# Optimization experiments

Measured on AMD Instinct MI355X. Metric: run time of the kernel, lower is better.

Reference implementation:

```python
import jax, jax.numpy as jnp
import numpy as np

B, N, D, H = 2, 256, 512, 8
DK = D // H


def _lin(x, w, b):
    # torch nn.Linear: y = x @ W.T + b, W is [out, in]
    return jnp.matmul(x, w.T) + b


def setup_inputs() -> dict:
    key = jax.random.key(0)
    ks = jax.random.split(key, 12)
    std = 0.02
    inp = {
        "x": jax.random.normal(ks[0], (B, N, D), jnp.float32),
        "batched_graphs": jax.random.normal(ks[1], (B, N, N, D), jnp.float32) * std,
        "mask": jnp.zeros((B, N, N), dtype=bool),
    }
    names = ["wq", "wk", "wv", "wo", "wl", "wr", "wrk", "wrv"]
    for i, n in enumerate(names):
        inp[n] = jax.random.normal(ks[2 + i], (D, D), jnp.float32) * std
        inp["b" + n[1:]] = jnp.zeros((D,), jnp.float32)
    return inp


def reference(x, batched_graphs, mask,
              wq, bq, wk, bk, wv, bv, wo, bo,
              wl, bl, wr, br, wrk, brk, wrv, brv):
    # update_relations: per-edge key/value maps
    graphs_k = _lin(batched_graphs, wrk, brk).reshape(B, N, N, H, DK)
    graphs_v = _lin(batched_graphs, wrv, brv).reshape(B, N, N, H, DK)

    query = _lin(x, wq, bq).reshape(B, N, H, DK)
    key_ = _lin(x, wk, bk).reshape(B, N, H, DK)
    value = _lin(x, wv, bv).reshape(B, N, H, DK)

    scores_k = jnp.einsum("bxhd,byhd->bxyh", query, key_)
    scores_g = jnp.einsum("bxhd,bxyhd->bxyh", query, graphs_k)
    scores = (scores_k + scores_g) / np.sqrt(DK).astype(np.float32)
    scores = jnp.where(mask[..., None], jnp.float32(-1e9), scores)
    p_attn = jax.nn.softmax(scores, axis=2)  # over key nodes y

    x_v = jnp.einsum("bxyh,byhd->bxhd", p_attn, value)
    x_g = jnp.einsum("bxyh,bxyhd->bxhd", p_attn, graphs_v)
    out = (x_v + x_g).reshape(B, N, D)

    # relation update: outer sum of left/right projections
    x_left = _lin(out, wl, bl)[:, :, None, :]   # [B,N,1,D]
    x_right = _lin(out, wr, br)[:, None, :, :]  # [B,1,N,D]
    new_graphs = x_left + x_right               # [B,N,N,D]

    return _lin(out, wo, bo), new_graphs
```

## Files before the change

### kernel.cpp

```cpp
#include <hip/hip_runtime.h>

#define BB 2
#define NN 256
#define DD 512
#define HH 8

typedef float f4raw __attribute__((ext_vector_type(4)));

__device__ __forceinline__ float dot4(float4 a, float4 b) {
    return a.x*b.x + a.y*b.y + a.z*b.z + a.w*b.w;
}

__device__ __forceinline__ float4 f4fma(float s, float4 a, float4 acc) {
    acc.x += s * a.x; acc.y += s * a.y; acc.z += s * a.z; acc.w += s * a.w;
    return acc;
}

__device__ __forceinline__ void gload_lds16(const void* g, void* l) {
    __builtin_amdgcn_global_load_lds(
        (const __attribute__((address_space(1))) unsigned int*)g,
        (__attribute__((address_space(3))) unsigned int*)l, 16, 0, 0);
}

__device__ __forceinline__ void stage_swz(const char* rowbase, float4* dst, int w, int lane) {
    #pragma unroll
    for (int j = 0; j < 4; ++j) {
        const int f0 = w * 256 + j * 64;
        const int y = f0 >> 7;
        const int c = (f0 & 127) + lane;
        gload_lds16(rowbase + (size_t)y * 2048 + ((size_t)(c ^ y) << 4), &dst[f0]);
    }
}

__global__ __launch_bounds__(256) void kProj(
    const float* __restrict__ in_,
    const float* __restrict__ w0, const float* __restrict__ b0,
    const float* __restrict__ w1, const float* __restrict__ b1,
    const float* __restrict__ w2, const float* __restrict__ b2,
    float* __restrict__ o0, float* __restrict__ o1, float* __restrict__ o2)
{
    __shared__ float4 xs[2][32 * 17];
    __shared__ float4 ws[2][32 * 17];

    const int t = threadIdx.x;
    const int blk = blockIdx.x;
    const int proj = blk >> 8;
    const int rem = blk & 255;
    const int row0 = (rem >> 4) * 32;
    const int col0 = (rem & 15) * 32;

    const float* W; const float* Bp; float* O;
    if (proj == 0)      { W = w0; Bp = b0; O = o0; }
    else if (proj == 1) { W = w1; Bp = b1; O = o1; }
    else                { W = w2; Bp = b2; O = o2; }

    const int sr0 = t >> 4,          se0 = t & 15;
    const int sr1 = (t + 256) >> 4,  se1 = t & 15;
    const float4* X4 = (const float4*)in_;
    const float4* W4 = (const float4*)W;

    float4 rx0 = X4[(size_t)(row0 + sr0) * 128 + se0];
    float4 rx1 = X4[(size_t)(row0 + sr1) * 128 + se1];
    float4 rw0 = W4[(size_t)(col0 + sr0) * 128 + se0];
    float4 rw1 = W4[(size_t)(col0 + sr1) * 128 + se1];
    xs[0][sr0 * 17 + se0] = rx0;
    xs[0][sr1 * 17 + se1] = rx1;
    ws[0][sr0 * 17 + se0] = rw0;
    ws[0][sr1 * 17 + se1] = rw1;

    const int ty = t >> 4, tx = t & 15;
    const int ra = 2 * ty, ca = 2 * tx;
    float a00 = 0, a01 = 0, a10 = 0, a11 = 0;

    for (int q = 0; q < 8; ++q) {
        __syncthreads();
        const int cur = q & 1;
        if (q < 7) {
            const int koff = (q + 1) * 16;
            rx0 = X4[(size_t)(row0 + sr0) * 128 + koff + se0];
            rx1 = X4[(size_t)(row0 + sr1) * 128 + koff + se1];
            rw0 = W4[(size_t)(col0 + sr0) * 128 + koff + se0];
            rw1 = W4[(size_t)(col0 + sr1) * 128 + koff + se1];
        }
        const float4* xb = xs[cur];
        const float4* wb = ws[cur];
        #pragma unroll
        for (int e4 = 0; e4 < 16; ++e4) {
            const float4 x0 = xb[ra * 17 + e4];
            const float4 x1 = xb[(ra + 1) * 17 + e4];
            const float4 v0 = wb[ca * 17 + e4];
            const float4 v1 = wb[(ca + 1) * 17 + e4];
            a00 += dot4(x0, v0); a01 += dot4(x0, v1);
            a10 += dot4(x1, v0); a11 += dot4(x1, v1);
        }
        if (q < 7) {
            const int nxt = cur ^ 1;
            xs[nxt][sr0 * 17 + se0] = rx0;
            xs[nxt][sr1 * 17 + se1] = rx1;
            ws[nxt][sr0 * 17 + se0] = rw0;
            ws[nxt][sr1 * 17 + se1] = rw1;
        }
    }

    const int orow = row0 + ra, ocol = col0 + ca;
    const float bx = Bp[ocol], by = Bp[ocol + 1];
    float2 s0; s0.x = a00 + bx; s0.y = a01 + by;
    float2 s1; s1.x = a10 + bx; s1.y = a11 + by;
    *(float2*)(O + (size_t)orow * DD + ocol) = s0;
    *(float2*)(O + (size_t)(orow + 1) * DD + ocol) = s1;
}

__global__ __launch_bounds__(256) void kQkp(
    const float* __restrict__ q, const float* __restrict__ wrk,
    float* __restrict__ qkp)
{
    __shared__ float qs[8 * 64];
    const int t = threadIdx.x;
    const int blk = blockIdx.x;
    const int rowg = blk >> 5;
    const int h = (blk >> 2) & 7;
    const int eq = blk & 3;
    const int row0 = rowg * 8;
    {
        const int r = t >> 5, d2 = (t & 31) * 2;
        const float2 tmp = *(const float2*)(q + (size_t)(row0 + r) * DD + h * 64 + d2);
        qs[r * 64 + d2] = tmp.x; qs[r * 64 + d2 + 1] = tmp.y;
    }
    __syncthreads();
    const int e = eq * 128 + (t & 127);
    const int rp = (t >> 7) * 4;
    const float* wcol = wrk + (size_t)(h * 64) * DD + e;
    float a0 = 0, a1 = 0, a2 = 0, a3 = 0;
    #pragma unroll 8
    for (int d = 0; d < 64; ++d) {
        const float wv = wcol[(size_t)d * DD];
        a0 += qs[(rp + 0) * 64 + d] * wv;
        a1 += qs[(rp + 1) * 64 + d] * wv;
        a2 += qs[(rp + 2) * 64 + d] * wv;
        a3 += qs[(rp + 3) * 64 + d] * wv;
    }
    qkp[((size_t)(row0 + rp + 0) * HH + h) * DD + e] = a0;
    qkp[((size_t)(row0 + rp + 1) * HH + h) * DD + e] = a1;
    qkp[((size_t)(row0 + rp + 2) * HH + h) * DD + e] = a2;
    qkp[((size_t)(row0 + rp + 3) * HH + h) * DD + e] = a3;
}

__global__ __launch_bounds__(256) void kSk(
    const float* __restrict__ q, const float* __restrict__ k,
    const unsigned char* __restrict__ mask, float* __restrict__ sk)
{
    __shared__ float qs[8 * 65];
    __shared__ float ks[64 * 65];
    const int t = threadIdx.x;
    const int blk = blockIdx.x;
    const int b  = blk >> 10;
    const int h  = (blk >> 7) & 7;
    const int xt = (blk >> 2) & 31;
    const int yt = blk & 3;
    const int x0 = xt * 8, y0 = yt * 64;
    {
        const int r = t >> 5, d2 = (t & 31) * 2;
        const float2 tmp = *(const float2*)(q + (size_t)(b * NN + x0 + r) * DD + h * 64 + d2);
        qs[r * 65 + d2] = tmp.x; qs[r * 65 + d2 + 1] = tmp.y;
    }
    #pragma unroll
    for (int j = 0; j < 8; ++j) {
        const int f = t + 256 * j;
        const int r = f >> 5, d2 = (f & 31) * 2;
        const float2 tmp = *(const float2*)(k + (size_t)(b * NN + y0 + r) * DD + h * 64 + d2);
        ks[r * 65 + d2] = tmp.x; ks[r * 65 + d2 + 1] = tmp.y;
    }
    __syncthreads();
    const int xi = t >> 5, yg = t & 31;
    float a0 = 0, a1 = 0;
    #pragma unroll 8
    for (int d = 0; d < 64; ++d) {
        const float qv = qs[xi * 65 + d];
        a0 += qv * ks[(yg * 2 + 0) * 65 + d];
        a1 += qv * ks[(yg * 2 + 1) * 65 + d];
    }
    a0 *= 0.125f; a1 *= 0.125f;
    const unsigned char* mrow = mask + (size_t)(b * NN + x0 + xi) * NN;
    const int gy = y0 + yg * 2;
    if (mrow[gy + 0]) a0 = -1e9f;
    if (mrow[gy + 1]) a1 = -1e9f;
    float2 st; st.x = a0; st.y = a1;
    *(float2*)(sk + ((size_t)(b * NN + x0 + xi) * HH + h) * NN + gy) = st;
}

__global__ __launch_bounds__(256) void kC(
    const float* __restrict__ G, const float* __restrict__ sk,
    const float* __restrict__ qkp, const float* __restrict__ v,
    float* __restrict__ pg, float* __restrict__ pxv,
    float* __restrict__ pm, float* __restrict__ pl)
{
    __shared__ float4 gbuf[2][1024];
    __shared__ float s_l[64];

    const int t = threadIdx.x;
    const int lane = t & 63;
    const int w = t >> 6;
    const int blk = blockIdx.x;
    const int part = blk & 3;
    const int bid = blk >> 2;
    const int b = bid >> 8;
    const int ybase = part * 64;

    const char* Grow = (const char*)(G + (size_t)bid * NN * DD);
    stage_swz(Grow + (size_t)ybase * 2048, &gbuf[0][0], w, lane);

    const int s_  = t & 15;
    const int h0i = ((t >> 4) & 3) * 2;
    const int y0i = w * 2;
    const int ec4 = t & 127;
    const int hb  = (t >> 7) * 4;
    const int hv  = t >> 5;
    const int d2  = (t & 31) * 2;
    const int ri  = hv & 3;

    const float* qkpb = qkp + (size_t)bid * HH * DD;
    float4 qv0[8], qv1[8];
    #pragma unroll
    for (int i = 0; i < 8; ++i) {
        const int e4 = i * 16 + s_;
        qv0[i] = *(const float4*)(qkpb + (size_t)h0i * DD + e4 * 4);
        qv1[i] = *(const float4*)(qkpb + (size_t)(h0i + 1) * DD + e4 * 4);
    }

    float4 gacc0 = {0,0,0,0}, gacc1 = {0,0,0,0}, gacc2 = {0,0,0,0}, gacc3 = {0,0,0,0};
    float m0 = -3e38f, m1 = -3e38f, m2 = -3e38f, m3 = -3e38f;
    float l0 = 0, l1 = 0, l2 = 0, l3 = 0;
    float vx = 0, vy = 0;

    const float* vrow = v + (size_t)(b * NN + ybase) * DD + hv * 64 + d2;
    const float* skrow = sk + (size_t)bid * HH * NN;

    __syncthreads();

    int cb = 0;
    for (int tt = 0; tt < 8; ++tt) {
        if (tt < 7)
            stage_swz(Grow + (size_t)(ybase + (tt + 1) * 8) * 2048, &gbuf[cb ^ 1][0], w, lane);

        float2 vvs[8];
        #pragma unroll
        for (int y = 0; y < 8; ++y)
            vvs[y] = *(const float2*)(vrow + ((size_t)tt * 8 + y) * DD);

        {
            float a00 = 0, a01 = 0, a10 = 0, a11 = 0;
            const float4* gb = &gbuf[cb][0];
            #pragma unroll
            for (int i = 0; i < 8; ++i) {
                const int e4 = i * 16 + s_;
                const float4 g0 = gb[y0i * 128 + (e4 ^ y0i)];
                const float4 g1 = gb[(y0i + 1) * 128 + (e4 ^ (y0i + 1))];
                a00 += dot4(g0, qv0[i]); a01 += dot4(g0, qv1[i]);
                a10 += dot4(g1, qv0[i]); a11 += dot4(g1, qv1[i]);
            }
            #pragma unroll
            for (int mm = 1; mm < 16; mm <<= 1) {
                a00 += __shfl_xor(a00, mm); a01 += __shfl_xor(a01, mm);
                a10 += __shfl_xor(a10, mm); a11 += __shfl_xor(a11, mm);
            }
            if (s_ < 4) {
                const int yy = s_ & 1, hh = s_ >> 1;
                const float val = yy ? (hh ? a11 : a10) : (hh ? a01 : a00);
                const int gy = ybase + tt * 8 + y0i + yy;
                const int h = h0i + hh;
                s_l[(y0i + yy) * 8 + h] = val * 0.125f + skrow[(size_t)h * NN + gy];
            }
        }
        __syncthreads();

        float4 sv[8];
        #pragma unroll
        for (int y = 0; y < 8; ++y) sv[y] = *(const float4*)&s_l[y * 8 + hb];

        float4 mx = sv[0];
        #pragma unroll
        for (int y = 1; y < 8; ++y) {
            mx.x = fmaxf(mx.x, sv[y].x); mx.y = fmaxf(mx.y, sv[y].y);
            mx.z = fmaxf(mx.z, sv[y].z); mx.w = fmaxf(mx.w, sv[y].w);
        }
        const float n0 = fmaxf(m0, mx.x), rs0 = __expf(m0 - n0);
        const float n1 = fmaxf(m1, mx.y), rs1 = __expf(m1 - n1);
        const float n2 = fmaxf(m2, mx.z), rs2 = __expf(m2 - n2);
        const float n3 = fmaxf(m3, mx.w), rs3 = __expf(m3 - n3);
        m0 = n0; m1 = n1; m2 = n2; m3 = n3;
        l0 *= rs0; l1 *= rs1; l2 *= rs2; l3 *= rs3;
        gacc0.x *= rs0; gacc0.y *= rs0; gacc0.z *= rs0; gacc0.w *= rs0;
        gacc1.x *= rs1; gacc1.y *= rs1; gacc1.z *= rs1; gacc1.w *= rs1;
        gacc2.x *= rs2; gacc2.y *= rs2; gacc2.z *= rs2; gacc2.w *= rs2;
        gacc3.x *= rs3; gacc3.y *= rs3; gacc3.z *= rs3; gacc3.w *= rs3;
        const float rsv = (ri == 0) ? rs0 : (ri == 1) ? rs1 : (ri == 2) ? rs2 : rs3;
        vx *= rsv; vy *= rsv;

        {
            const float4* gb = &gbuf[cb][0];
            #pragma unroll
            for (int y = 0; y < 8; ++y) {
                const float4 gv = gb[y * 128 + (ec4 ^ y)];
                const float4 s = sv[y];
                const float p0 = __expf(s.x - m0); l0 += p0; gacc0 = f4fma(p0, gv, gacc0);
                const float p1 = __expf(s.y - m1); l1 += p1; gacc1 = f4fma(p1, gv, gacc1);
                const float p2 = __expf(s.z - m2); l2 += p2; gacc2 = f4fma(p2, gv, gacc2);
                const float p3 = __expf(s.w - m3); l3 += p3; gacc3 = f4fma(p3, gv, gacc3);
                const float pv = (ri == 0) ? p0 : (ri == 1) ? p1 : (ri == 2) ? p2 : p3;
                vx += pv * vvs[y].x; vy += pv * vvs[y].y;
            }
        }
        __syncthreads();
        cb ^= 1;
    }

    float4* pgb = (float4*)pg + (size_t)blk * 1024;
    pgb[(hb + 0) * 128 + ec4] = gacc0;
    pgb[(hb + 1) * 128 + ec4] = gacc1;
    pgb[(hb + 2) * 128 + ec4] = gacc2;
    pgb[(hb + 3) * 128 + ec4] = gacc3;
    float2 xvst; xvst.x = vx; xvst.y = vy;
    *(float2*)(pxv + (size_t)blk * DD + hv * 64 + d2) = xvst;
    if ((t & 127) == 0) {
        const int base = blk * 8 + hb;
        pm[base + 0] = m0; pm[base + 1] = m1; pm[base + 2] = m2; pm[base + 3] = m3;
        pl[base + 0] = l0; pl[base + 1] = l1; pl[base + 2] = l2; pl[base + 3] = l3;
    }
}

__global__ __launch_bounds__(256) void kM(
    const float* __restrict__ pg, const float* __restrict__ pxv,
    const float* __restrict__ pm, const float* __restrict__ pl,
    const float* __restrict__ wrv, const float* __restrict__ brv,
    float* __restrict__ om)
{
    __shared__ float4 gc[512];
    __shared__ float xvs[256];
    __shared__ float wexp[16], Ls[4];
    const int t = threadIdx.x;
    const int blk = blockIdx.x;
    const int bid = blk >> 1;
    const int half = blk & 1;
    const int h0 = half * 4;
    __shared__ float mlds[16], llds[16];
    if (t < 16) {
        const int i = t >> 2, hh = t & 3;
        mlds[t] = pm[bid * 32 + i * 8 + h0 + hh];
        llds[t] = pl[bid * 32 + i * 8 + h0 + hh];
    }
    __syncthreads();
    if (t < 4) {
        float M = mlds[t];
        #pragma unroll
        for (int i = 1; i < 4; ++i) M = fmaxf(M, mlds[i * 4 + t]);
        float L = 0;
        #pragma unroll
        for (int i = 0; i < 4; ++i) {
            const float wv = __expf(mlds[i * 4 + t] - M);
            wexp[i * 4 + t] = wv;
            L += wv * llds[i * 4 + t];
        }
        Ls[t] = L;
    }
    __syncthreads();
    const int c4 = t & 127;
    #pragma unroll
    for (int r = 0; r < 2; ++r) {
        const int hh = (t >> 7) * 2 + r;
        float4 acc = {0, 0, 0, 0};
        #pragma unroll
        for (int i = 0; i < 4; ++i) {
            const float wv = wexp[i * 4 + hh];
            const float4 g = ((const float4*)pg)[((size_t)bid * 4 + i) * 1024 + (size_t)(h0 + hh) * 128 + c4];
            acc.x += wv * g.x; acc.y += wv * g.y; acc.z += wv * g.z; acc.w += wv * g.w;
        }
        gc[hh * 128 + c4] = acc;
    }
    {
        const int hh = t >> 6;
        float s = 0;
        #pragma unroll
        for (int i = 0; i < 4; ++i)
            s += wexp[i * 4 + hh] * pxv[((size_t)bid * 4 + i) * DD + half * 256 + t];
        xvs[t] = s;
    }
    __syncthreads();
    const int o = half * 256 + t;
    const int hl = t >> 6;
    const float4* wr4 = (const float4*)(wrv + (size_t)o * DD);
    float acc = 0;
    #pragma unroll 4
    for (int e4 = 0; e4 < 128; ++e4) acc += dot4(wr4[e4], gc[hl * 128 + e4]);
    om[(size_t)bid * DD + o] = (xvs[t] + acc) / Ls[hl] + brv[o];
}

__global__ __launch_bounds__(256) void kE(
    const float* __restrict__ xl, const float* __restrict__ xr,
    float* __restrict__ ng)
{
    const int t = threadIdx.x;
    const int blk = blockIdx.x;
    const int bid = blk >> 2;
    const int yc = blk & 3;
    const int b = bid >> 8;
    const int o4 = t & 127;
    const int yh = t >> 7;
    const float4 left = ((const float4*)xl)[(size_t)bid * 128 + o4];
    const float4* xr4 = (const float4*)xr + (size_t)b * NN * 128;
    f4raw* out4 = (f4raw*)ng + (size_t)bid * NN * 128;
    for (int y = yc * 64 + yh; y < yc * 64 + 64; y += 2) {
        const float4 rr = xr4[y * 128 + o4];
        f4raw s;
        s.x = left.x + rr.x; s.y = left.y + rr.y;
        s.z = left.z + rr.z; s.w = left.w + rr.w;
        __builtin_nontemporal_store(s, &out4[y * 128 + o4]);
    }
}

extern "C" void kernel_launch(void* const* d_in, const int* in_sizes, int n_in,
                              void* d_out, int out_size, void* d_ws, size_t ws_size,
                              hipStream_t stream)
{
    (void)in_sizes; (void)n_in; (void)out_size; (void)ws_size;
    const float* x    = (const float*)d_in[0];
    const float* G    = (const float*)d_in[1];
    const unsigned char* mask = (const unsigned char*)d_in[2];
    const float* wq  = (const float*)d_in[3];  const float* bq  = (const float*)d_in[4];
    const float* wk  = (const float*)d_in[5];  const float* bk  = (const float*)d_in[6];
    const float* wv  = (const float*)d_in[7];  const float* bv  = (const float*)d_in[8];
    const float* wo  = (const float*)d_in[9];  const float* bo  = (const float*)d_in[10];
    const float* wl  = (const float*)d_in[11]; const float* bl  = (const float*)d_in[12];
    const float* wr  = (const float*)d_in[13]; const float* br  = (const float*)d_in[14];
    const float* wrk = (const float*)d_in[15];
    const float* wrv = (const float*)d_in[17]; const float* brv = (const float*)d_in[18];

    float* out  = (float*)d_out;
    float* fout = out;
    float* ng   = out + (size_t)BB * NN * DD;

    const size_t ng_f  = (size_t)BB * NN * NN * DD;
    const size_t row_f = (size_t)BB * NN * DD;
    const size_t total = row_f * 52 + 32768;
    float* base = ng + ng_f - total;
    float* q    = base;
    float* k    = q   + row_f;
    float* vv_  = k   + row_f;
    float* qkp  = vv_ + row_f;
    float* skp  = qkp + row_f * 8;
    float* pg   = skp + row_f * 4;
    float* pxv  = pg  + row_f * 32;
    float* pm   = pxv + row_f * 4;
    float* pl   = pm  + 16384;
    float* om   = pl  + 16384;
    float* xl = (float*)d_ws;
    float* xr = xl + row_f;

    kProj<<<768, 256, 0, stream>>>(x, wq, bq, wk, bk, wv, bv, q, k, vv_);
    kQkp <<<2048, 256, 0, stream>>>(q, wrk, qkp);
    kSk  <<<2048, 256, 0, stream>>>(q, k, mask, skp);
    kC   <<<2048, 256, 0, stream>>>(G, skp, qkp, vv_, pg, pxv, pm, pl);
    kM   <<<1024, 256, 0, stream>>>(pg, pxv, pm, pl, wrv, brv, om);
    kProj<<<768, 256, 0, stream>>>(om, wo, bo, wl, bl, wr, br, fout, xl, xr);
    kE   <<<2048, 256, 0, stream>>>(xl, xr, ng);
}
```

Before: 297.0 us.

## Fuse split-softmax merge and wrv projection into single-block-per-row attention kernel

The graph-attention kernel kC now uses one 512-thread block per query row and walks all 256 key nodes, instead of four partial blocks whose results a separate kM kernel merged. The wrv projection and normalisation move into kC's epilogue, which removes the partial-result buffers, the global round trip and one launch. kProj is also rewritten as a 64-thread block that computes a 4x4 register tile per thread. The risk is lower parallelism in kC (512 blocks instead of 2048) and a longer serial loop per block.

```diff
diff --git a/kernel.cpp b/kernel.cpp
--- a/kernel.cpp
+++ b/kernel.cpp
@@ -22,25 +22,25 @@
         (__attribute__((address_space(3))) unsigned int*)l, 16, 0, 0);
 }
 
-__device__ __forceinline__ void stage_swz(const char* rowbase, float4* dst, int w, int lane) {
+__device__ __forceinline__ void stage_swz8(const char* rowbase, float4* dst, int w, int lane) {
     #pragma unroll
-    for (int j = 0; j < 4; ++j) {
-        const int f0 = w * 256 + j * 64;
-        const int y = f0 >> 7;
-        const int c = (f0 & 127) + lane;
+    for (int j = 0; j < 2; ++j) {
+        const int f0 = w * 128 + j * 64;
+        const int y = w;
+        const int c = j * 64 + lane;
         gload_lds16(rowbase + (size_t)y * 2048 + ((size_t)(c ^ y) << 4), &dst[f0]);
     }
 }
 
-__global__ __launch_bounds__(256) void kProj(
+__global__ __launch_bounds__(64) void kProj(
     const float* __restrict__ in_,
     const float* __restrict__ w0, const float* __restrict__ b0,
     const float* __restrict__ w1, const float* __restrict__ b1,
     const float* __restrict__ w2, const float* __restrict__ b2,
     float* __restrict__ o0, float* __restrict__ o1, float* __restrict__ o2)
 {
-    __shared__ float4 xs[2][32 * 17];
-    __shared__ float4 ws[2][32 * 17];
+    __shared__ float4 xs[2][32 * 5];
+    __shared__ float4 ws[2][32 * 5];
 
     const int t = threadIdx.x;
     const int blk = blockIdx.x;
@@ -54,60 +54,63 @@
     else if (proj == 1) { W = w1; Bp = b1; O = o1; }
     else                { W = w2; Bp = b2; O = o2; }
 
-    const int sr0 = t >> 4,          se0 = t & 15;
-    const int sr1 = (t + 256) >> 4,  se1 = t & 15;
-    const float4* X4 = (const float4*)in_;
-    const float4* W4 = (const float4*)W;
-
-    float4 rx0 = X4[(size_t)(row0 + sr0) * 128 + se0];
-    float4 rx1 = X4[(size_t)(row0 + sr1) * 128 + se1];
-    float4 rw0 = W4[(size_t)(col0 + sr0) * 128 + se0];
-    float4 rw1 = W4[(size_t)(col0 + sr1) * 128 + se1];
-    xs[0][sr0 * 17 + se0] = rx0;
-    xs[0][sr1 * 17 + se1] = rx1;
-    ws[0][sr0 * 17 + se0] = rw0;
-    ws[0][sr1 * 17 + se1] = rw1;
-
-    const int ty = t >> 4, tx = t & 15;
-    const int ra = 2 * ty, ca = 2 * tx;
-    float a00 = 0, a01 = 0, a10 = 0, a11 = 0;
-
-    for (int q = 0; q < 8; ++q) {
+    const float4* X4 = (const float4*)in_ + (size_t)row0 * 128;
+    const float4* W4 = (const float4*)W  + (size_t)col0 * 128;
+
+    const int sr = t >> 2, se = t & 3;
+    const int ty = t >> 3, tx = t & 7;
+
+    float4 rx0 = X4[(size_t)sr * 128 + se];
+    float4 rx1 = X4[(size_t)(sr + 16) * 128 + se];
+    float4 rw0 = W4[(size_t)sr * 128 + se];
+    float4 rw1 = W4[(size_t)(sr + 16) * 128 + se];
+    xs[0][sr * 5 + se] = rx0;  xs[0][(sr + 16) * 5 + se] = rx1;
+    ws[0][sr * 5 + se] = rw0;  ws[0][(sr + 16) * 5 + se] = rw1;
+
+    float acc[4][4] = {};
+
+    for (int q = 0; q < 32; ++q) {
         __syncthreads();
         const int cur = q & 1;
-        if (q < 7) {
-            const int koff = (q + 1) * 16;
-            rx0 = X4[(size_t)(row0 + sr0) * 128 + koff + se0];
-            rx1 = X4[(size_t)(row0 + sr1) * 128 + koff + se1];
-            rw0 = W4[(size_t)(col0 + sr0) * 128 + koff + se0];
-            rw1 = W4[(size_t)(col0 + sr1) * 128 + koff + se1];
+        if (q < 31) {
+            const int ko = (q + 1) * 4;
+            rx0 = X4[(size_t)sr * 128 + ko + se];
+            rx1 = X4[(size_t)(sr + 16) * 128 + ko + se];
+            rw0 = W4[(size_t)sr * 128 + ko + se];
+            rw1 = W4[(size_t)(sr + 16) * 128 + ko + se];
         }
         const float4* xb = xs[cur];
         const float4* wb = ws[cur];
         #pragma unroll
-        for (int e4 = 0; e4 < 16; ++e4) {
-            const float4 x0 = xb[ra * 17 + e4];
-            const float4 x1 = xb[(ra + 1) * 17 + e4];
-            const float4 v0 = wb[ca * 17 + e4];
-            const float4 v1 = wb[(ca + 1) * 17 + e4];
-            a00 += dot4(x0, v0); a01 += dot4(x0, v1);
-            a10 += dot4(x1, v0); a11 += dot4(x1, v1);
-        }
-        if (q < 7) {
+        for (int e4 = 0; e4 < 4; ++e4) {
+            float4 xr[4], wc[4];
+            #pragma unroll
+            for (int i = 0; i < 4; ++i) xr[i] = xb[(ty + 8 * i) * 5 + e4];
+            #pragma unroll
+            for (int j = 0; j < 4; ++j) wc[j] = wb[(tx + 8 * j) * 5 + e4];
+            #pragma unroll
+            for (int i = 0; i < 4; ++i)
+                #pragma unroll
+                for (int j = 0; j < 4; ++j)
+                    acc[i][j] += dot4(xr[i], wc[j]);
+        }
+        if (q < 31) {
             const int nxt = cur ^ 1;
-            xs[nxt][sr0 * 17 + se0] = rx0;
-            xs[nxt][sr1 * 17 + se1] = rx1;
-            ws[nxt][sr0 * 17 + se0] = rw0;
-            ws[nxt][sr1 * 17 + se1] = rw1;
-        }
-    }
-
-    const int orow = row0 + ra, ocol = col0 + ca;
-    const float bx = Bp[ocol], by = Bp[ocol + 1];
-    float2 s0; s0.x = a00 + bx; s0.y = a01 + by;
-    float2 s1; s1.x = a10 + bx; s1.y = a11 + by;
-    *(float2*)(O + (size_t)orow * DD + ocol) = s0;
-    *(float2*)(O + (size_t)(orow + 1) * DD + ocol) = s1;
+            xs[nxt][sr * 5 + se] = rx0;  xs[nxt][(sr + 16) * 5 + se] = rx1;
+            ws[nxt][sr * 5 + se] = rw0;  ws[nxt][(sr + 16) * 5 + se] = rw1;
+        }
+    }
+
+    float bb[4];
+    #pragma unroll
+    for (int j = 0; j < 4; ++j) bb[j] = Bp[col0 + tx + 8 * j];
+    #pragma unroll
+    for (int i = 0; i < 4; ++i) {
+        const int orow = row0 + ty + 8 * i;
+        #pragma unroll
+        for (int j = 0; j < 4; ++j)
+            O[(size_t)orow * DD + col0 + tx + 8 * j] = acc[i][j] + bb[j];
+    }
 }
 
 __global__ __launch_bounds__(256) void kQkp(
@@ -188,210 +191,131 @@
     *(float2*)(sk + ((size_t)(b * NN + x0 + xi) * HH + h) * NN + gy) = st;
 }
 
-__global__ __launch_bounds__(256) void kC(
+__global__ __launch_bounds__(512) void kC(
     const float* __restrict__ G, const float* __restrict__ sk,
     const float* __restrict__ qkp, const float* __restrict__ v,
-    float* __restrict__ pg, float* __restrict__ pxv,
-    float* __restrict__ pm, float* __restrict__ pl)
+    const float* __restrict__ wrv, const float* __restrict__ brv,
+    float* __restrict__ om)
 {
     __shared__ float4 gbuf[2][1024];
+    __shared__ float4 qgc[1024];
     __shared__ float s_l[64];
+    __shared__ float lL[8];
+    __shared__ float xvs[512];
 
     const int t = threadIdx.x;
     const int lane = t & 63;
     const int w = t >> 6;
-    const int blk = blockIdx.x;
-    const int part = blk & 3;
-    const int bid = blk >> 2;
+    const int bid = blockIdx.x;
     const int b = bid >> 8;
-    const int ybase = part * 64;
 
     const char* Grow = (const char*)(G + (size_t)bid * NN * DD);
-    stage_swz(Grow + (size_t)ybase * 2048, &gbuf[0][0], w, lane);
+    stage_swz8((const char*)(qkp + (size_t)bid * HH * DD), qgc, w, lane);
+    stage_swz8(Grow, &gbuf[0][0], w, lane);
 
     const int s_  = t & 15;
-    const int h0i = ((t >> 4) & 3) * 2;
-    const int y0i = w * 2;
+    const int sg  = t >> 4;
+    const int sy  = sg >> 2;
+    const int h0i = (sg & 3) * 2;
     const int ec4 = t & 127;
-    const int hb  = (t >> 7) * 4;
-    const int hv  = t >> 5;
-    const int d2  = (t & 31) * 2;
-    const int ri  = hv & 3;
-
-    const float* qkpb = qkp + (size_t)bid * HH * DD;
-    float4 qv0[8], qv1[8];
-    #pragma unroll
-    for (int i = 0; i < 8; ++i) {
-        const int e4 = i * 16 + s_;
-        qv0[i] = *(const float4*)(qkpb + (size_t)h0i * DD + e4 * 4);
-        qv1[i] = *(const float4*)(qkpb + (size_t)(h0i + 1) * DD + e4 * 4);
-    }
-
-    float4 gacc0 = {0,0,0,0}, gacc1 = {0,0,0,0}, gacc2 = {0,0,0,0}, gacc3 = {0,0,0,0};
-    float m0 = -3e38f, m1 = -3e38f, m2 = -3e38f, m3 = -3e38f;
-    float l0 = 0, l1 = 0, l2 = 0, l3 = 0;
-    float vx = 0, vy = 0;
-
-    const float* vrow = v + (size_t)(b * NN + ybase) * DD + hv * 64 + d2;
+    const int hb  = (t >> 7) * 2;
+    const int hv  = t >> 6;
+    const int dv  = t & 63;
+    const int ri  = hv & 1;
+
+    float4 gacc0 = {0,0,0,0}, gacc1 = {0,0,0,0};
+    float m0 = -3e38f, m1 = -3e38f, l0 = 0, l1 = 0, vx = 0;
+
+    const float* vcol = v + (size_t)(b * NN) * DD + hv * 64 + dv;
     const float* skrow = sk + (size_t)bid * HH * NN;
 
     __syncthreads();
 
     int cb = 0;
-    for (int tt = 0; tt < 8; ++tt) {
-        if (tt < 7)
-            stage_swz(Grow + (size_t)(ybase + (tt + 1) * 8) * 2048, &gbuf[cb ^ 1][0], w, lane);
-
-        float2 vvs[8];
-        #pragma unroll
-        for (int y = 0; y < 8; ++y)
-            vvs[y] = *(const float2*)(vrow + ((size_t)tt * 8 + y) * DD);
+    for (int tt = 0; tt < 32; ++tt) {
+        if (tt < 31)
+            stage_swz8(Grow + (size_t)(tt + 1) * 8 * 2048, &gbuf[cb ^ 1][0], w, lane);
+
+        float vvs[8];
+        #pragma unroll
+        for (int y = 0; y < 8; ++y) vvs[y] = vcol[((size_t)tt * 8 + y) * DD];
 
         {
-            float a00 = 0, a01 = 0, a10 = 0, a11 = 0;
+            float a0 = 0, a1 = 0;
             const float4* gb = &gbuf[cb][0];
             #pragma unroll
             for (int i = 0; i < 8; ++i) {
                 const int e4 = i * 16 + s_;
-                const float4 g0 = gb[y0i * 128 + (e4 ^ y0i)];
-                const float4 g1 = gb[(y0i + 1) * 128 + (e4 ^ (y0i + 1))];
-                a00 += dot4(g0, qv0[i]); a01 += dot4(g0, qv1[i]);
-                a10 += dot4(g1, qv0[i]); a11 += dot4(g1, qv1[i]);
+                const float4 g0 = gb[sy * 128 + (e4 ^ sy)];
+                a0 += dot4(g0, qgc[h0i * 128 + (e4 ^ h0i)]);
+                a1 += dot4(g0, qgc[(h0i + 1) * 128 + (e4 ^ (h0i + 1))]);
             }
             #pragma unroll
             for (int mm = 1; mm < 16; mm <<= 1) {
-                a00 += __shfl_xor(a00, mm); a01 += __shfl_xor(a01, mm);
-                a10 += __shfl_xor(a10, mm); a11 += __shfl_xor(a11, mm);
+                a0 += __shfl_xor(a0, mm); a1 += __shfl_xor(a1, mm);
             }
-            if (s_ < 4) {
-                const int yy = s_ & 1, hh = s_ >> 1;
-                const float val = yy ? (hh ? a11 : a10) : (hh ? a01 : a00);
-                const int gy = ybase + tt * 8 + y0i + yy;
-                const int h = h0i + hh;
-                s_l[(y0i + yy) * 8 + h] = val * 0.125f + skrow[(size_t)h * NN + gy];
+            if (s_ < 2) {
+                const float val = (s_ == 0) ? a0 : a1;
+                const int h = h0i + s_;
+                const int gy = tt * 8 + sy;
+                s_l[sy * 8 + h] = val * 0.125f + skrow[(size_t)h * NN + gy];
             }
         }
         __syncthreads();
 
-        float4 sv[8];
-        #pragma unroll
-        for (int y = 0; y < 8; ++y) sv[y] = *(const float4*)&s_l[y * 8 + hb];
-
-        float4 mx = sv[0];
+        float2 sv[8];
+        #pragma unroll
+        for (int y = 0; y < 8; ++y) sv[y] = *(const float2*)&s_l[y * 8 + hb];
+
+        float mx0 = sv[0].x, mx1 = sv[0].y;
         #pragma unroll
         for (int y = 1; y < 8; ++y) {
-            mx.x = fmaxf(mx.x, sv[y].x); mx.y = fmaxf(mx.y, sv[y].y);
-            mx.z = fmaxf(mx.z, sv[y].z); mx.w = fmaxf(mx.w, sv[y].w);
-        }
-        const float n0 = fmaxf(m0, mx.x), rs0 = __expf(m0 - n0);
-        const float n1 = fmaxf(m1, mx.y), rs1 = __expf(m1 - n1);
-        const float n2 = fmaxf(m2, mx.z), rs2 = __expf(m2 - n2);
-        const float n3 = fmaxf(m3, mx.w), rs3 = __expf(m3 - n3);
-        m0 = n0; m1 = n1; m2 = n2; m3 = n3;
-        l0 *= rs0; l1 *= rs1; l2 *= rs2; l3 *= rs3;
+            mx0 = fmaxf(mx0, sv[y].x); mx1 = fmaxf(mx1, sv[y].y);
+        }
+        const float n0 = fmaxf(m0, mx0), rs0 = __expf(m0 - n0);
+        const float n1 = fmaxf(m1, mx1), rs1 = __expf(m1 - n1);
+        m0 = n0; m1 = n1;
+        l0 *= rs0; l1 *= rs1;
         gacc0.x *= rs0; gacc0.y *= rs0; gacc0.z *= rs0; gacc0.w *= rs0;
         gacc1.x *= rs1; gacc1.y *= rs1; gacc1.z *= rs1; gacc1.w *= rs1;
-        gacc2.x *= rs2; gacc2.y *= rs2; gacc2.z *= rs2; gacc2.w *= rs2;
-        gacc3.x *= rs3; gacc3.y *= rs3; gacc3.z *= rs3; gacc3.w *= rs3;
-        const float rsv = (ri == 0) ? rs0 : (ri == 1) ? rs1 : (ri == 2) ? rs2 : rs3;
-        vx *= rsv; vy *= rsv;
+        vx *= ri ? rs1 : rs0;
 
         {
             const float4* gb = &gbuf[cb][0];
             #pragma unroll
             for (int y = 0; y < 8; ++y) {
                 const float4 gv = gb[y * 128 + (ec4 ^ y)];
-                const float4 s = sv[y];
-                const float p0 = __expf(s.x - m0); l0 += p0; gacc0 = f4fma(p0, gv, gacc0);
-                const float p1 = __expf(s.y - m1); l1 += p1; gacc1 = f4fma(p1, gv, gacc1);
-                const float p2 = __expf(s.z - m2); l2 += p2; gacc2 = f4fma(p2, gv, gacc2);
-                const float p3 = __expf(s.w - m3); l3 += p3; gacc3 = f4fma(p3, gv, gacc3);
-                const float pv = (ri == 0) ? p0 : (ri == 1) ? p1 : (ri == 2) ? p2 : p3;
-                vx += pv * vvs[y].x; vy += pv * vvs[y].y;
+                const float p0 = __expf(sv[y].x - m0); l0 += p0; gacc0 = f4fma(p0, gv, gacc0);
+                const float p1 = __expf(sv[y].y - m1); l1 += p1; gacc1 = f4fma(p1, gv, gacc1);
+                vx += (ri ? p1 : p0) * vvs[y];
             }
         }
         __syncthreads();
         cb ^= 1;
     }
 
-    float4* pgb = (float4*)pg + (size_t)blk * 1024;
-    pgb[(hb + 0) * 128 + ec4] = gacc0;
-    pgb[(hb + 1) * 128 + ec4] = gacc1;
-    pgb[(hb + 2) * 128 + ec4] = gacc2;
-    pgb[(hb + 3) * 128 + ec4] = gacc3;
-    float2 xvst; xvst.x = vx; xvst.y = vy;
-    *(float2*)(pxv + (size_t)blk * DD + hv * 64 + d2) = xvst;
-    if ((t & 127) == 0) {
-        const int base = blk * 8 + hb;
-        pm[base + 0] = m0; pm[base + 1] = m1; pm[base + 2] = m2; pm[base + 3] = m3;
-        pl[base + 0] = l0; pl[base + 1] = l1; pl[base + 2] = l2; pl[base + 3] = l3;
-    }
-}
-
-__global__ __launch_bounds__(256) void kM(
-    const float* __restrict__ pg, const float* __restrict__ pxv,
-    const float* __restrict__ pm, const float* __restrict__ pl,
-    const float* __restrict__ wrv, const float* __restrict__ brv,
-    float* __restrict__ om)
-{
-    __shared__ float4 gc[512];
-    __shared__ float xvs[256];
-    __shared__ float wexp[16], Ls[4];
-    const int t = threadIdx.x;
-    const int blk = blockIdx.x;
-    const int bid = blk >> 1;
-    const int half = blk & 1;
-    const int h0 = half * 4;
-    __shared__ float mlds[16], llds[16];
-    if (t < 16) {
-        const int i = t >> 2, hh = t & 3;
-        mlds[t] = pm[bid * 32 + i * 8 + h0 + hh];
-        llds[t] = pl[bid * 32 + i * 8 + h0 + hh];
-    }
+    qgc[(hb + 0) * 128 + ec4] = gacc0;
+    qgc[(hb + 1) * 128 + ec4] = gacc1;
+    if (ec4 == 0) { lL[hb] = l0; lL[hb + 1] = l1; }
+    xvs[hv * 64 + dv] = vx;
     __syncthreads();
-    if (t < 4) {
-        float M = mlds[t];
-        #pragma unroll
-        for (int i = 1; i < 4; ++i) M = fmaxf(M, mlds[i * 4 + t]);
-        float L = 0;
-        #pragma unroll
-        for (int i = 0; i < 4; ++i) {
-            const float wv = __expf(mlds[i * 4 + t] - M);
-            wexp[i * 4 + t] = wv;
-            L += wv * llds[i * 4 + t];
-        }
-        Ls[t] = L;
-    }
-    __syncthreads();
-    const int c4 = t & 127;
-    #pragma unroll
-    for (int r = 0; r < 2; ++r) {
-        const int hh = (t >> 7) * 2 + r;
-        float4 acc = {0, 0, 0, 0};
-        #pragma unroll
-        for (int i = 0; i < 4; ++i) {
-            const float wv = wexp[i * 4 + hh];
-            const float4 g = ((const float4*)pg)[((size_t)bid * 4 + i) * 1024 + (size_t)(h0 + hh) * 128 + c4];
-            acc.x += wv * g.x; acc.y += wv * g.y; acc.z += wv * g.z; acc.w += wv * g.w;
-        }
-        gc[hh * 128 + c4] = acc;
-    }
-    {
-        const int hh = t >> 6;
-        float s = 0;
-        #pragma unroll
-        for (int i = 0; i < 4; ++i)
-            s += wexp[i * 4 + hh] * pxv[((size_t)bid * 4 + i) * DD + half * 256 + t];
-        xvs[t] = s;
-    }
-    __syncthreads();
-    const int o = half * 256 + t;
-    const int hl = t >> 6;
-    const float4* wr4 = (const float4*)(wrv + (size_t)o * DD);
-    float acc = 0;
-    #pragma unroll 4
-    for (int e4 = 0; e4 < 128; ++e4) acc += dot4(wr4[e4], gc[hl * 128 + e4]);
-    om[(size_t)bid * DD + o] = (xvs[t] + acc) / Ls[hl] + brv[o];
+
+    #pragma unroll 2
+    for (int oo = 0; oo < 16; ++oo) {
+        const int o = sg * 16 + oo;
+        const int ho = o >> 6;
+        const float4* wr4 = (const float4*)(wrv + (size_t)o * DD);
+        float acc = 0;
+        #pragma unroll
+        for (int i = 0; i < 8; ++i) {
+            const int e4 = i * 16 + s_;
+            acc += dot4(wr4[e4], qgc[ho * 128 + e4]);
+        }
+        #pragma unroll
+        for (int mm = 1; mm < 16; mm <<= 1) acc += __shfl_xor(acc, mm);
+        if (s_ == 0)
+            om[(size_t)bid * DD + o] = (xvs[o] + acc) / lL[ho] + brv[o];
+    }
 }
 
 __global__ __launch_bounds__(256) void kE(
@@ -440,26 +364,21 @@
 
     const size_t ng_f  = (size_t)BB * NN * NN * DD;
     const size_t row_f = (size_t)BB * NN * DD;
-    const size_t total = row_f * 52 + 32768;
+    const size_t total = row_f * 17;
     float* base = ng + ng_f - total;
     float* q    = base;
     float* k    = q   + row_f;
     float* vv_  = k   + row_f;
     float* qkp  = vv_ + row_f;
     float* skp  = qkp + row_f * 8;
-    float* pg   = skp + row_f * 4;
-    float* pxv  = pg  + row_f * 32;
-    float* pm   = pxv + row_f * 4;
-    float* pl   = pm  + 16384;
-    float* om   = pl  + 16384;
+    float* om   = skp + row_f * 4;
     float* xl = (float*)d_ws;
     float* xr = xl + row_f;
 
-    kProj<<<768, 256, 0, stream>>>(x, wq, bq, wk, bk, wv, bv, q, k, vv_);
+    kProj<<<768, 64, 0, stream>>>(x, wq, bq, wk, bk, wv, bv, q, k, vv_);
     kQkp <<<2048, 256, 0, stream>>>(q, wrk, qkp);
     kSk  <<<2048, 256, 0, stream>>>(q, k, mask, skp);
-    kC   <<<2048, 256, 0, stream>>>(G, skp, qkp, vv_, pg, pxv, pm, pl);
-    kM   <<<1024, 256, 0, stream>>>(pg, pxv, pm, pl, wrv, brv, om);
-    kProj<<<768, 256, 0, stream>>>(om, wo, bo, wl, bl, wr, br, fout, xl, xr);
+    kC   <<<512, 512, 0, stream>>>(G, skp, qkp, vv_, wrv, brv, om);
+    kProj<<<768, 64, 0, stream>>>(om, wo, bo, wl, bl, wr, br, fout, xl, xr);
     kE   <<<2048, 256, 0, stream>>>(xl, xr, ng);
 }
```

Measured after the change: 305.7 us. +2.9%, slower.
